# Kernel tuning notes

Hardware: AMD Instinct MI355X
Metric: run time of the kernel (lower is better)

## Reference

```python
import jax, jax.numpy as jnp
import numpy as np

D_PROJ = 256
SCALE = D_PROJ ** (-0.5)


def setup_inputs() -> dict:
    key = jax.random.key(0)
    k1, k2, k3, k4 = jax.random.split(key, 4)
    B, L, Dh = 16, 2048, 1280
    T, Dg = 512, 768
    H = jax.random.normal(k1, (B, L, Dh), dtype=jnp.float32)
    G = jax.random.normal(k2, (B, T, Dg), dtype=jnp.float32)
    # Linear weights (torch nn.Linear: out = x @ W.T), small init to keep softmax well-conditioned
    Wq = jax.random.normal(k3, (D_PROJ, Dg), dtype=jnp.float32) * 0.02
    Wk = jax.random.normal(k4, (D_PROJ, Dh), dtype=jnp.float32) * 0.02
    return {"H": H, "G": G, "Wq": Wq, "Wk": Wk}


def reference(H, G, Wq, Wk):
    # Q = Wq(G): [B,T,P]; K = Wk(H): [B,L,P]
    Q = jnp.einsum('btg,pg->btp', G, Wq)
    K = jnp.einsum('bld,pd->blp', H, Wk)
    # The torch module's chunked online-softmax computes exact softmax over L.
    logits = jnp.einsum('btp,blp->btl', Q, K) * SCALE  # [B,T,L]
    A = jax.nn.softmax(logits, axis=-1)
    # Values are the raw residue embeddings H (not projected).
    Z = jnp.einsum('btl,bld->btd', A, H)  # [B,T,Dh]
    return Z
```

## Files before the change

### kernel.cpp

```cpp
#include <hip/hip_runtime.h>
#include <stdint.h>

typedef __attribute__((ext_vector_type(8))) short   short8;
typedef __attribute__((ext_vector_type(8))) __bf16  bf16x8;
typedef __attribute__((ext_vector_type(4))) float   floatx4;

#define DEV static __device__ __forceinline__

DEV unsigned short f2b(float f) {
  union { float f; unsigned u; } v; v.f = f;
  unsigned u = v.u;
  unsigned r = u + 0x7FFFu + ((u >> 16) & 1u);
  return (unsigned short)(r >> 16);
}

DEV void gload_lds16(const void* g, void* l) {
  __builtin_amdgcn_global_load_lds(
      (const __attribute__((address_space(1))) unsigned int*)g,
      (__attribute__((address_space(3))) unsigned int*)l,
      16, 0, 0);
}

__global__ void cvtw_kernel(const float* __restrict__ a, unsigned short* __restrict__ oa, int na4,
                            const float* __restrict__ b, unsigned short* __restrict__ ob, int nb4,
                            float* __restrict__ zp, int nz) {
  int i = blockIdx.x * blockDim.x + threadIdx.x;
  if (i < na4) {
    float4 v = ((const float4*)a)[i];
    ushort4 o; o.x = f2b(v.x); o.y = f2b(v.y); o.z = f2b(v.z); o.w = f2b(v.w);
    ((ushort4*)oa)[i] = o;
  } else if (i < na4 + nb4) {
    int k = i - na4;
    float4 v = ((const float4*)b)[k];
    ushort4 o; o.x = f2b(v.x); o.y = f2b(v.y); o.z = f2b(v.z); o.w = f2b(v.w);
    ((ushort4*)ob)[k] = o;
  } else if (i < na4 + nb4 + nz) {
    zp[i - na4 - nb4] = 0.f;
  }
}

template <int WRITE_HT>
__global__ void proj_gemm(const float* __restrict__ A32, const unsigned short* __restrict__ Bt,
                          unsigned short* __restrict__ C, unsigned short* __restrict__ HT,
                          int K, int lda) {
  __shared__ unsigned short As[64 * 32];
  __shared__ unsigned short Bs[256 * 32];
  __shared__ unsigned short At2[WRITE_HT ? 32 * 66 : 1];

  const int m0   = blockIdx.x * 64;
  const int t    = threadIdx.x;
  const int lane = t & 63;
  const int wave = t >> 6;
  const int wn   = wave * 64;
  const int r16  = lane & 15;
  const int q    = lane >> 4;

  floatx4 acc[4][4];
#pragma unroll
  for (int i = 0; i < 4; ++i)
#pragma unroll
    for (int j = 0; j < 4; ++j) acc[i][j] = (floatx4){0.f, 0.f, 0.f, 0.f};

  for (int kt = 0; kt < K; kt += 32) {
    __syncthreads();
#pragma unroll
    for (int cc = 0; cc < 4; ++cc) {
      int c = t + cc * 256;
      gload_lds16(Bt + (size_t)(c >> 2) * K + kt + (c & 3) * 8, &Bs[c * 8]);
    }
    {
      const int row = t >> 2;
      const int seg = t & 3;
      const float* g = A32 + (size_t)(m0 + row) * lda + kt + seg * 8;
      float4 v0 = *(const float4*)g;
      float4 v1 = *(const float4*)(g + 4);
      short8 p;
      p[0] = (short)f2b(v0.x); p[1] = (short)f2b(v0.y);
      p[2] = (short)f2b(v0.z); p[3] = (short)f2b(v0.w);
      p[4] = (short)f2b(v1.x); p[5] = (short)f2b(v1.y);
      p[6] = (short)f2b(v1.z); p[7] = (short)f2b(v1.w);
      *(short8*)&As[t * 8] = p;
      if constexpr (WRITE_HT) {
#pragma unroll
        for (int j = 0; j < 8; ++j)
          At2[(seg * 8 + j) * 66 + row] = (unsigned short)p[j];
      }
    }
    __syncthreads();

    bf16x8 af[4], bfr[4];
#pragma unroll
    for (int i = 0; i < 4; ++i) af[i]  = *(const bf16x8*)&As[(i * 16 + r16) * 32 + q * 8];
#pragma unroll
    for (int j = 0; j < 4; ++j) bfr[j] = *(const bf16x8*)&Bs[(wn + j * 16 + r16) * 32 + q * 8];
#pragma unroll
    for (int i = 0; i < 4; ++i)
#pragma unroll
      for (int j = 0; j < 4; ++j)
        acc[i][j] = __builtin_amdgcn_mfma_f32_16x16x32_bf16(af[i], bfr[j], acc[i][j], 0, 0, 0);

    if constexpr (WRITE_HT) {
      const int d  = t >> 3;
      const int lc = t & 7;
      const unsigned* w = (const unsigned*)At2 + d * 33 + lc * 4;
      union { unsigned u[4]; short8 s; } vv;
      vv.u[0] = w[0]; vv.u[1] = w[1]; vv.u[2] = w[2]; vv.u[3] = w[3];
      const int b  = m0 >> 11;
      const int l0 = m0 & 2047;
      *(short8*)&HT[((size_t)b * 1280 + kt + d) * 2048 + l0 + lc * 8] = vv.s;
    }
  }

#pragma unroll
  for (int i = 0; i < 4; ++i) {
#pragma unroll
    for (int r = 0; r < 4; ++r) {
      int m = m0 + i * 16 + q * 4 + r;
#pragma unroll
      for (int j = 0; j < 4; ++j) {
        int n = wn + j * 16 + r16;
        C[(size_t)m * 256 + n] = f2b(acc[i][j][r]);
      }
    }
  }
}

template <int EPI>
__global__ void gemm_nt(const unsigned short* __restrict__ Ab, const unsigned short* __restrict__ Btb,
                        void* __restrict__ Cpv, float* __restrict__ sums,
                        int K, int lda, int ldb, int ldc,
                        long long sA, long long sB, long long sC, int sstride,
                        float escale, int nx, int tiles_pb) {
  __shared__ unsigned short As[128 * 32];
  __shared__ unsigned short Bs[128 * 32];

  const int g   = blockIdx.x;
  const int xcd = g & 7;
  const int jj  = g >> 3;
  const int bz  = xcd * 2 + jj / tiles_pb;
  const int tt  = jj % tiles_pb;
  const int m0  = (tt / nx) * 128;
  const int n0  = (tt % nx) * 128;

  const int t    = threadIdx.x;
  const int lane = t & 63;
  const int wave = t >> 6;
  const int wm   = (wave & 1) * 64;
  const int wn   = (wave >> 1) * 64;
  const int r16  = lane & 15;
  const int q    = lane >> 4;

  const unsigned short* Bt = Btb + (long long)bz * sB;
  const unsigned short* A  = Ab + (long long)bz * sA;

  floatx4 acc[4][4];
#pragma unroll
  for (int i = 0; i < 4; ++i)
#pragma unroll
    for (int j = 0; j < 4; ++j) acc[i][j] = (floatx4){0.f, 0.f, 0.f, 0.f};

  for (int kt = 0; kt < K; kt += 32) {
    __syncthreads();
#pragma unroll
    for (int cc = 0; cc < 2; ++cc) {
      int c = t + cc * 256;
      gload_lds16(Bt + (size_t)(n0 + (c >> 2)) * ldb + kt + (c & 3) * 8, &Bs[c * 8]);
    }
#pragma unroll
    for (int cc = 0; cc < 2; ++cc) {
      int c = t + cc * 256;
      gload_lds16(A + (size_t)(m0 + (c >> 2)) * lda + kt + (c & 3) * 8, &As[c * 8]);
    }
    __syncthreads();

    bf16x8 af[4], bfr[4];
#pragma unroll
    for (int i = 0; i < 4; ++i) af[i]  = *(const bf16x8*)&As[(wm + i * 16 + r16) * 32 + q * 8];
#pragma unroll
    for (int j = 0; j < 4; ++j) bfr[j] = *(const bf16x8*)&Bs[(wn + j * 16 + r16) * 32 + q * 8];
#pragma unroll
    for (int i = 0; i < 4; ++i)
#pragma unroll
      for (int j = 0; j < 4; ++j)
        acc[i][j] = __builtin_amdgcn_mfma_f32_16x16x32_bf16(af[i], bfr[j], acc[i][j], 0, 0, 0);
  }

  if constexpr (EPI == 1) {
    unsigned short* C = (unsigned short*)Cpv + (long long)bz * sC;
#pragma unroll
    for (int i = 0; i < 4; ++i) {
#pragma unroll
      for (int r = 0; r < 4; ++r) {
        int m = m0 + wm + i * 16 + q * 4 + r;
        float ps = 0.f;
#pragma unroll
        for (int j = 0; j < 4; ++j) {
          int n = n0 + wn + j * 16 + r16;
          float v = __expf(acc[i][j][r] * escale);
          ps += v;
          C[(size_t)m * ldc + n] = f2b(v);
        }
#pragma unroll
        for (int msk = 1; msk < 16; msk <<= 1) ps += __shfl_xor(ps, msk, 64);
        if (r16 == 0) atomicAdd(&sums[(long long)bz * sstride + m], ps);
      }
    }
  } else {
    float* C = (float*)Cpv + (long long)bz * sC;
    const float* sb = sums + (long long)bz * sstride;
#pragma unroll
    for (int i = 0; i < 4; ++i) {
#pragma unroll
      for (int r = 0; r < 4; ++r) {
        int m = m0 + wm + i * 16 + q * 4 + r;
        float sc = 1.0f / sb[m];
#pragma unroll
        for (int j = 0; j < 4; ++j) {
          int n = n0 + wn + j * 16 + r16;
          C[(size_t)m * ldc + n] = acc[i][j][r] * sc;
        }
      }
    }
  }
}

extern "C" void kernel_launch(void* const* d_in, const int* in_sizes, int n_in,
                              void* d_out, int out_size, void* d_ws, size_t ws_size,
                              hipStream_t stream) {
  (void)in_sizes; (void)n_in; (void)out_size; (void)ws_size;
  const float* H  = (const float*)d_in[0];
  const float* G  = (const float*)d_in[1];
  const float* Wq = (const float*)d_in[2];
  const float* Wk = (const float*)d_in[3];
  float* Z = (float*)d_out;

  constexpr int B = 16, L = 2048, Dh = 1280, T = 512, Dg = 768, P = 256;

  char* ws = (char*)d_ws;
  size_t off = 0;
  auto alloc = [&](size_t bytes) { void* p = ws + off; off += (bytes + 255) & ~(size_t)255; return p; };
  unsigned short* Wqbf = (unsigned short*)alloc((size_t)P * Dg * 2);
  unsigned short* Wkbf = (unsigned short*)alloc((size_t)P * Dh * 2);
  unsigned short* Qbf  = (unsigned short*)alloc((size_t)B * T * P * 2);
  unsigned short* Kbf  = (unsigned short*)alloc((size_t)B * L * P * 2);
  unsigned short* HT   = (unsigned short*)alloc((size_t)B * Dh * L * 2);
  unsigned short* E    = (unsigned short*)alloc((size_t)B * T * L * 2);
  float*          sums = (float*)alloc((size_t)B * T * 4);

  {
    int na4 = P * Dg / 4, nb4 = P * Dh / 4, nz = B * T;
    cvtw_kernel<<<(na4 + nb4 + nz + 255) / 256, 256, 0, stream>>>(
        Wq, Wqbf, na4, Wk, Wkbf, nb4, sums, nz);
  }

  proj_gemm<0><<<B * T / 64, 256, 0, stream>>>(G, Wqbf, Qbf, nullptr, Dg, Dg);
  proj_gemm<1><<<B * L / 64, 256, 0, stream>>>(H, Wkbf, Kbf, HT, Dh, Dh);

  gemm_nt<1><<<B * (T / 128) * (L / 128), 256, 0, stream>>>(
      Qbf, Kbf, E, sums, P, P, P, L,
      (long long)T * P, (long long)L * P, (long long)T * L, T,
      0.0625f, L / 128, (T / 128) * (L / 128));

  gemm_nt<2><<<B * (T / 128) * (Dh / 128), 256, 0, stream>>>(
      E, HT, Z, sums, L, L, L, Dh,
      (long long)T * L, (long long)Dh * L, (long long)T * Dh, T,
      0.f, Dh / 128, (T / 128) * (Dh / 128));
}
```

Before: 412.7 us.

## Double-buffer weight tiles and prefetch activations in projection GEMM with 512 threads

The projection GEMM now runs 512 threads as 8 waves in a 2x4 grid, each computing a 32x64 sub-tile instead of 64x64. The weight tile goes into a double-buffered LDS array and the next K-step's weights and fp32 activation rows are issued before the MFMAs, so global loads overlap compute. The aim is to hide load latency in the H projection, which also writes the transposed HT copy. The cost is more LDS, smaller per-wave tiles with more B-fragment reads, and narrower HT stores.

```diff
diff --git a/kernel.cpp b/kernel.cpp
--- a/kernel.cpp
+++ b/kernel.cpp
@@ -40,82 +40,93 @@
 }
 
 template <int WRITE_HT>
-__global__ void proj_gemm(const float* __restrict__ A32, const unsigned short* __restrict__ Bt,
-                          unsigned short* __restrict__ C, unsigned short* __restrict__ HT,
-                          int K, int lda) {
+__global__ __launch_bounds__(512) void proj_gemm(
+    const float* __restrict__ A32, const unsigned short* __restrict__ Bt,
+    unsigned short* __restrict__ C, unsigned short* __restrict__ HT,
+    int K, int lda) {
   __shared__ unsigned short As[64 * 32];
-  __shared__ unsigned short Bs[256 * 32];
+  __shared__ unsigned short Bs[2][256 * 32];
   __shared__ unsigned short At2[WRITE_HT ? 32 * 66 : 1];
 
   const int m0   = blockIdx.x * 64;
   const int t    = threadIdx.x;
   const int lane = t & 63;
   const int wave = t >> 6;
-  const int wn   = wave * 64;
+  const int wm   = (wave & 1) * 32;
+  const int wn   = (wave >> 1) * 64;
   const int r16  = lane & 15;
   const int q    = lane >> 4;
 
-  floatx4 acc[4][4];
-#pragma unroll
-  for (int i = 0; i < 4; ++i)
+  const int arow = t >> 3;
+  const int aseg = t & 7;
+  const float* ag = A32 + (size_t)(m0 + arow) * lda + aseg * 4;
+
+  floatx4 acc[2][4];
+#pragma unroll
+  for (int i = 0; i < 2; ++i)
 #pragma unroll
     for (int j = 0; j < 4; ++j) acc[i][j] = (floatx4){0.f, 0.f, 0.f, 0.f};
 
+#pragma unroll
+  for (int cc = 0; cc < 2; ++cc) {
+    int c = t + cc * 512;
+    gload_lds16(Bt + (size_t)(c >> 2) * K + (c & 3) * 8, &Bs[0][c * 8]);
+  }
+  float4 v = *(const float4*)ag;
+
   for (int kt = 0; kt < K; kt += 32) {
-    __syncthreads();
-#pragma unroll
-    for (int cc = 0; cc < 4; ++cc) {
-      int c = t + cc * 256;
-      gload_lds16(Bt + (size_t)(c >> 2) * K + kt + (c & 3) * 8, &Bs[c * 8]);
-    }
-    {
-      const int row = t >> 2;
-      const int seg = t & 3;
-      const float* g = A32 + (size_t)(m0 + row) * lda + kt + seg * 8;
-      float4 v0 = *(const float4*)g;
-      float4 v1 = *(const float4*)(g + 4);
-      short8 p;
-      p[0] = (short)f2b(v0.x); p[1] = (short)f2b(v0.y);
-      p[2] = (short)f2b(v0.z); p[3] = (short)f2b(v0.w);
-      p[4] = (short)f2b(v1.x); p[5] = (short)f2b(v1.y);
-      p[6] = (short)f2b(v1.z); p[7] = (short)f2b(v1.w);
-      *(short8*)&As[t * 8] = p;
-      if constexpr (WRITE_HT) {
-#pragma unroll
-        for (int j = 0; j < 8; ++j)
-          At2[(seg * 8 + j) * 66 + row] = (unsigned short)p[j];
-      }
-    }
-    __syncthreads();
-
-    bf16x8 af[4], bfr[4];
-#pragma unroll
-    for (int i = 0; i < 4; ++i) af[i]  = *(const bf16x8*)&As[(i * 16 + r16) * 32 + q * 8];
-#pragma unroll
-    for (int j = 0; j < 4; ++j) bfr[j] = *(const bf16x8*)&Bs[(wn + j * 16 + r16) * 32 + q * 8];
-#pragma unroll
-    for (int i = 0; i < 4; ++i)
+    const int cur = (kt >> 5) & 1;
+    __syncthreads();
+
+    ushort4 pv;
+    pv.x = f2b(v.x); pv.y = f2b(v.y); pv.z = f2b(v.z); pv.w = f2b(v.w);
+    *(ushort4*)&As[t * 4] = pv;
+    if constexpr (WRITE_HT) {
+      At2[(aseg * 4 + 0) * 66 + arow] = pv.x;
+      At2[(aseg * 4 + 1) * 66 + arow] = pv.y;
+      At2[(aseg * 4 + 2) * 66 + arow] = pv.z;
+      At2[(aseg * 4 + 3) * 66 + arow] = pv.w;
+    }
+    __syncthreads();
+
+    if (kt + 32 < K) {
+#pragma unroll
+      for (int cc = 0; cc < 2; ++cc) {
+        int c = t + cc * 512;
+        gload_lds16(Bt + (size_t)(c >> 2) * K + (kt + 32) + (c & 3) * 8,
+                    &Bs[cur ^ 1][c * 8]);
+      }
+      v = *(const float4*)(ag + kt + 32);
+    }
+
+    bf16x8 af[2], bfr[4];
+#pragma unroll
+    for (int i = 0; i < 2; ++i) af[i]  = *(const bf16x8*)&As[(wm + i * 16 + r16) * 32 + q * 8];
+#pragma unroll
+    for (int j = 0; j < 4; ++j) bfr[j] = *(const bf16x8*)&Bs[cur][(wn + j * 16 + r16) * 32 + q * 8];
+#pragma unroll
+    for (int i = 0; i < 2; ++i)
 #pragma unroll
       for (int j = 0; j < 4; ++j)
         acc[i][j] = __builtin_amdgcn_mfma_f32_16x16x32_bf16(af[i], bfr[j], acc[i][j], 0, 0, 0);
 
     if constexpr (WRITE_HT) {
-      const int d  = t >> 3;
-      const int lc = t & 7;
-      const unsigned* w = (const unsigned*)At2 + d * 33 + lc * 4;
-      union { unsigned u[4]; short8 s; } vv;
-      vv.u[0] = w[0]; vv.u[1] = w[1]; vv.u[2] = w[2]; vv.u[3] = w[3];
+      const int d  = t >> 4;
+      const int lc = t & 15;
+      const unsigned* w = (const unsigned*)At2 + d * 33 + lc * 2;
+      union { unsigned u[2]; ushort4 s; } vv;
+      vv.u[0] = w[0]; vv.u[1] = w[1];
       const int b  = m0 >> 11;
       const int l0 = m0 & 2047;
-      *(short8*)&HT[((size_t)b * 1280 + kt + d) * 2048 + l0 + lc * 8] = vv.s;
-    }
-  }
-
-#pragma unroll
-  for (int i = 0; i < 4; ++i) {
+      *(ushort4*)&HT[((size_t)b * 1280 + kt + d) * 2048 + l0 + lc * 4] = vv.s;
+    }
+  }
+
+#pragma unroll
+  for (int i = 0; i < 2; ++i) {
 #pragma unroll
     for (int r = 0; r < 4; ++r) {
-      int m = m0 + i * 16 + q * 4 + r;
+      int m = m0 + wm + i * 16 + q * 4 + r;
 #pragma unroll
       for (int j = 0; j < 4; ++j) {
         int n = wn + j * 16 + r16;
@@ -253,8 +264,8 @@
         Wq, Wqbf, na4, Wk, Wkbf, nb4, sums, nz);
   }
 
-  proj_gemm<0><<<B * T / 64, 256, 0, stream>>>(G, Wqbf, Qbf, nullptr, Dg, Dg);
-  proj_gemm<1><<<B * L / 64, 256, 0, stream>>>(H, Wkbf, Kbf, HT, Dh, Dh);
+  proj_gemm<0><<<B * T / 64, 512, 0, stream>>>(G, Wqbf, Qbf, nullptr, Dg, Dg);
+  proj_gemm<1><<<B * L / 64, 512, 0, stream>>>(H, Wkbf, Kbf, HT, Dh, Dh);
 
   gemm_nt<1><<<B * (T / 128) * (L / 128), 256, 0, stream>>>(
       Qbf, Kbf, E, sums, P, P, P, L,
```

Measured after the change: 447.0 us. 8.3% more time.

## Double-buffer projection GEMM with async global-to-LDS loads for fp32 A and B

Applied to the files above, without the earlier changes.

The projection GEMM now stages fp32 A tiles and bf16 B tiles into double-buffered LDS with direct global-to-LDS loads issued two iterations ahead, synchronised with explicit vmcnt waits and barriers. The fp32-to-bf16 conversion now reads from LDS instead of from synchronous global loads, so memory latency overlaps the MFMA work. In exchange, LDS use grows considerably (fp32 A buffers), which may reduce occupancy, and the hand-written waitcnt logic is fragile.

```diff
diff --git a/kernel.cpp b/kernel.cpp
--- a/kernel.cpp
+++ b/kernel.cpp
@@ -40,11 +40,13 @@
 }
 
 template <int WRITE_HT>
-__global__ void proj_gemm(const float* __restrict__ A32, const unsigned short* __restrict__ Bt,
-                          unsigned short* __restrict__ C, unsigned short* __restrict__ HT,
-                          int K, int lda) {
+__global__ __launch_bounds__(256) void proj_gemm(
+    const float* __restrict__ A32, const unsigned short* __restrict__ Bt,
+    unsigned short* __restrict__ C, unsigned short* __restrict__ HT,
+    int K, int lda) {
+  __shared__ float          Af32[2][64 * 32];
+  __shared__ unsigned short Bs[2][256 * 32];
   __shared__ unsigned short As[64 * 32];
-  __shared__ unsigned short Bs[256 * 32];
   __shared__ unsigned short At2[WRITE_HT ? 32 * 66 : 1];
 
   const int m0   = blockIdx.x * 64;
@@ -54,6 +56,7 @@
   const int wn   = wave * 64;
   const int r16  = lane & 15;
   const int q    = lane >> 4;
+  const int nt   = K >> 5;
 
   floatx4 acc[4][4];
 #pragma unroll
@@ -61,50 +64,82 @@
 #pragma unroll
     for (int j = 0; j < 4; ++j) acc[i][j] = (floatx4){0.f, 0.f, 0.f, 0.f};
 
-  for (int kt = 0; kt < K; kt += 32) {
-    __syncthreads();
+  auto stage = [&](int it, int buf) {
+    const int kt = it << 5;
+#pragma unroll
+    for (int cc = 0; cc < 2; ++cc) {
+      int c = t + cc * 256;
+      gload_lds16(A32 + (size_t)(m0 + (c >> 3)) * lda + kt + (c & 7) * 4,
+                  &Af32[buf][c * 4]);
+    }
 #pragma unroll
     for (int cc = 0; cc < 4; ++cc) {
       int c = t + cc * 256;
-      gload_lds16(Bt + (size_t)(c >> 2) * K + kt + (c & 3) * 8, &Bs[c * 8]);
-    }
+      gload_lds16(Bt + (size_t)(c >> 2) * K + kt + (c & 3) * 8, &Bs[buf][c * 8]);
+    }
+  };
+
+  stage(0, 0);
+  stage(1, 1);
+
+  for (int it = 0; it < nt; ++it) {
+    const int cur = it & 1;
+    const int kt  = it << 5;
+
+    if (it == nt - 1) { asm volatile("s_waitcnt vmcnt(0)" ::: "memory"); }
+    else              { asm volatile("s_waitcnt vmcnt(6)" ::: "memory"); }
+    __builtin_amdgcn_sched_barrier(0);
+
     {
-      const int row = t >> 2;
-      const int seg = t & 3;
-      const float* g = A32 + (size_t)(m0 + row) * lda + kt + seg * 8;
-      float4 v0 = *(const float4*)g;
-      float4 v1 = *(const float4*)(g + 4);
-      short8 p;
-      p[0] = (short)f2b(v0.x); p[1] = (short)f2b(v0.y);
-      p[2] = (short)f2b(v0.z); p[3] = (short)f2b(v0.w);
-      p[4] = (short)f2b(v1.x); p[5] = (short)f2b(v1.y);
-      p[6] = (short)f2b(v1.z); p[7] = (short)f2b(v1.w);
-      *(short8*)&As[t * 8] = p;
+      const int row = t >> 3;
+      const int kc  = t & 7;
+      float4 v0 = *(const float4*)&Af32[cur][t * 4];
+      float4 v1 = *(const float4*)&Af32[cur][t * 4 + 1024];
+      unsigned short e0[4], e1[4];
+      e0[0] = f2b(v0.x); e0[1] = f2b(v0.y); e0[2] = f2b(v0.z); e0[3] = f2b(v0.w);
+      e1[0] = f2b(v1.x); e1[1] = f2b(v1.y); e1[2] = f2b(v1.z); e1[3] = f2b(v1.w);
+      ushort4 p0, p1;
+      p0.x = e0[0]; p0.y = e0[1]; p0.z = e0[2]; p0.w = e0[3];
+      p1.x = e1[0]; p1.y = e1[1]; p1.z = e1[2]; p1.w = e1[3];
+      *(ushort4*)&As[row * 32 + kc * 4]        = p0;
+      *(ushort4*)&As[(row + 32) * 32 + kc * 4] = p1;
       if constexpr (WRITE_HT) {
 #pragma unroll
-        for (int j = 0; j < 8; ++j)
-          At2[(seg * 8 + j) * 66 + row] = (unsigned short)p[j];
+        for (int jj = 0; jj < 4; ++jj) {
+          At2[(kc * 4 + jj) * 66 + row]      = e0[jj];
+          At2[(kc * 4 + jj) * 66 + row + 32] = e1[jj];
+        }
       }
     }
-    __syncthreads();
+    asm volatile("s_waitcnt lgkmcnt(0)\n\ts_barrier" ::: "memory");
+    __builtin_amdgcn_sched_barrier(0);
 
     bf16x8 af[4], bfr[4];
 #pragma unroll
     for (int i = 0; i < 4; ++i) af[i]  = *(const bf16x8*)&As[(i * 16 + r16) * 32 + q * 8];
 #pragma unroll
-    for (int j = 0; j < 4; ++j) bfr[j] = *(const bf16x8*)&Bs[(wn + j * 16 + r16) * 32 + q * 8];
-#pragma unroll
-    for (int i = 0; i < 4; ++i)
-#pragma unroll
-      for (int j = 0; j < 4; ++j)
-        acc[i][j] = __builtin_amdgcn_mfma_f32_16x16x32_bf16(af[i], bfr[j], acc[i][j], 0, 0, 0);
-
+    for (int j = 0; j < 4; ++j) bfr[j] = *(const bf16x8*)&Bs[cur][(wn + j * 16 + r16) * 32 + q * 8];
+    union { unsigned u[4]; short8 s; } vv;
     if constexpr (WRITE_HT) {
       const int d  = t >> 3;
       const int lc = t & 7;
       const unsigned* w = (const unsigned*)At2 + d * 33 + lc * 4;
-      union { unsigned u[4]; short8 s; } vv;
       vv.u[0] = w[0]; vv.u[1] = w[1]; vv.u[2] = w[2]; vv.u[3] = w[3];
+    }
+    asm volatile("s_waitcnt lgkmcnt(0)\n\ts_barrier" ::: "memory");
+    __builtin_amdgcn_sched_barrier(0);
+
+    if (it + 2 < nt) stage(it + 2, cur);
+
+#pragma unroll
+    for (int i = 0; i < 4; ++i)
+#pragma unroll
+      for (int j = 0; j < 4; ++j)
+        acc[i][j] = __builtin_amdgcn_mfma_f32_16x16x32_bf16(af[i], bfr[j], acc[i][j], 0, 0, 0);
+
+    if constexpr (WRITE_HT) {
+      const int d  = t >> 3;
+      const int lc = t & 7;
       const int b  = m0 >> 11;
       const int l0 = m0 & 2047;
       *(short8*)&HT[((size_t)b * 1280 + kt + d) * 2048 + l0 + lc * 8] = vv.s;
```

Result: no change. 410.9 us (-0.5%).
